# Performance work log

Hardware: AMD Instinct MI355X
Metric: run time of the kernel (lower is better)

The kernel has to match this reference:

```python
import jax, jax.numpy as jnp
import numpy as np

B, N, H, E = 8, 256, 128, 32

def setup_inputs() -> dict:
    key = jax.random.key(0)
    ks = jax.random.split(key, 9)
    x = jax.random.normal(ks[0], (B, N, H), dtype=jnp.float32)
    adj = jax.random.randint(ks[1], (B, N, N), 0, 2, dtype=jnp.int32)
    e = jax.random.normal(ks[2], (B, N, N, E), dtype=jnp.float32)
    s = 0.02
    We = jax.random.normal(ks[3], (E, H), dtype=jnp.float32) * s
    be = jax.random.normal(ks[4], (H,), dtype=jnp.float32) * s
    W1 = jax.random.normal(ks[5], (H, 2 * H), dtype=jnp.float32) * s
    b1 = jax.random.normal(ks[6], (2 * H,), dtype=jnp.float32) * s
    W2 = jax.random.normal(ks[7], (2 * H, H), dtype=jnp.float32) * s
    b2 = jax.random.normal(ks[8], (H,), dtype=jnp.float32) * s
    return {"x": x, "adj": adj, "e": e, "We": We, "be": be,
            "W1": W1, "b1": b1, "W2": W2, "b2": b2}

def reference(x, adj, e, We, be, W1, b1, W2, b2):
    # edge projection: [B,N,N,E] -> [B,N,N,H]
    e_h = jnp.einsum('bije,eh->bijh', e, We) + be
    # message m[b,i,j] = relu(x[b,j] + e_h[b,i,j]); mask by adj
    m = jax.nn.relu(x[:, None, :, :] + e_h)
    m = jnp.where((adj != 0)[..., None], m, jnp.zeros((), m.dtype))
    agg = m.sum(axis=2)  # sum over j -> [B,N,H]
    h = agg + x
    out = jax.nn.relu(h @ W1 + b1) @ W2 + b2
    return out
```

## Files before the change

kernel.cpp:

```cpp
#include <hip/hip_runtime.h>
#include <hip/hip_bf16.h>

#define B_ 8
#define N_ 256
#define H_ 128
#define E_ 32
#define XLS_STRIDE 264

typedef __bf16 bf16x8 __attribute__((ext_vector_type(8)));
typedef __bf16 bf16x4 __attribute__((ext_vector_type(4)));
typedef float f32x4 __attribute__((ext_vector_type(4)));

static __device__ __forceinline__ __bf16 f2bf(float f) {
    union { float f; unsigned int u; } a;
    a.f = f;
    const unsigned int r = a.u + 0x7FFFu + ((a.u >> 16) & 1u);
    union { unsigned short s; __bf16 b; } o;
    o.s = (unsigned short)(r >> 16);
    return o.b;
}

#define W1T_OFF  131072
#define W2T_OFF  163840
#define WEBF_OFF 196608

__global__ __launch_bounds__(256) void prep_kernel(
    const float* __restrict__ x, const float* __restrict__ be,
    const float* __restrict__ W1, const float* __restrict__ W2,
    const float* __restrict__ We, float* __restrict__ ws)
{
    const int blk = blockIdx.x;
    if (blk == 320) {
        __bf16* Webf = (__bf16*)(ws + WEBF_OFF);
        for (int q = threadIdx.x; q < 512; q += 256) {
            const int quad = q >> 7, h = q & 127;
            bf16x8 t;
#pragma unroll
            for (int kk = 0; kk < 8; ++kk)
                t[kk] = f2bf(We[(quad * 8 + kk) * H_ + h]);
            *(bf16x8*)&Webf[q * 8] = t;
        }
        return;
    }
    __shared__ float tile[32][33];
    const int tx = threadIdx.x & 31, ty = threadIdx.x >> 5;
    if (blk < 256) {
        const int b = blk >> 5, t = blk & 31;
        const float* src = x + (size_t)b * N_ * H_;
        __bf16* dst = (__bf16*)ws + (size_t)b * H_ * N_;
        const int r0 = (t >> 2) * 32, c0 = (t & 3) * 32;
#pragma unroll
        for (int p = 0; p < 4; ++p)
            tile[ty + p * 8][tx] =
                src[(size_t)(r0 + ty + p * 8) * H_ + c0 + tx] + be[c0 + tx];
        __syncthreads();
#pragma unroll
        for (int p = 0; p < 4; ++p)
            dst[(size_t)(c0 + ty + p * 8) * N_ + r0 + tx] = f2bf(tile[tx][ty + p * 8]);
        return;
    }
    const float* src; float* dst; int R, C, r0, c0;
    if (blk < 288) {
        const int t = blk - 256;
        src = W1; dst = ws + W1T_OFF;
        R = 128; C = 256; r0 = (t >> 3) * 32; c0 = (t & 7) * 32;
    } else {
        const int t = blk - 288;
        src = W2; dst = ws + W2T_OFF;
        R = 256; C = 128; r0 = (t >> 2) * 32; c0 = (t & 3) * 32;
    }
#pragma unroll
    for (int p = 0; p < 4; ++p)
        tile[ty + p * 8][tx] = src[(size_t)(r0 + ty + p * 8) * C + c0 + tx];
    __syncthreads();
#pragma unroll
    for (int p = 0; p < 4; ++p)
        dst[(size_t)(c0 + ty + p * 8) * R + r0 + tx] = tile[tx][ty + p * 8];
}

__global__ __launch_bounds__(256, 2) void agg_kernel(
    const int* __restrict__ adj, const float* __restrict__ e,
    const float* __restrict__ ws, const float* __restrict__ x,
    float* __restrict__ hout)
{
    __shared__ __bf16 xls[H_ * XLS_STRIDE];
    __shared__ float red[4][128];
    const int bi   = blockIdx.x;
    const int b    = bi >> 8;
    const int tid  = threadIdx.x;
    const int w    = tid >> 6;
    const int lane = tid & 63;
    const int quad = lane >> 4;
    const int col  = lane & 15;

    const size_t ebase   = (size_t)bi * (N_ * E_);
    const size_t adjbase = (size_t)bi * N_;

    float4 a0v[2], a1v[2];
    int4   avv[2];
#pragma unroll
    for (int p = 0; p < 2; ++p) {
        const int j0 = (p * 4 + w) * 16;
        const float* ap = e + ebase + (size_t)(j0 + col) * E_ + quad * 8;
        a0v[p] = *(const float4*)ap;
        a1v[p] = *(const float4*)(ap + 4);
        avv[p] = *(const int4*)(adj + adjbase + j0 + quad * 4);
    }

    {
        const __bf16* gx = (const __bf16*)ws + (size_t)b * (H_ * N_);
#pragma unroll 4
        for (int it = 0; it < 16; ++it) {
            const int k   = it * 256 + tid;
            const int row = k >> 5, cc = k & 31;
            const f32x4 v = *(const f32x4*)(gx + (size_t)row * 256 + cc * 8);
            *(f32x4*)&xls[row * XLS_STRIDE + cc * 8] = v;
        }
    }

    const __bf16* Webf = (const __bf16*)(ws + WEBF_OFF);
    bf16x8 bw[8];
#pragma unroll
    for (int ht = 0; ht < 8; ++ht)
        bw[ht] = *(const bf16x8*)&Webf[(quad * 128 + ht * 16 + col) * 8];

    float psum[8];
#pragma unroll
    for (int ht = 0; ht < 8; ++ht) psum[ht] = 0.0f;

    const f32x4 zero4 = {0.0f, 0.0f, 0.0f, 0.0f};

    __syncthreads();

#pragma unroll
    for (int c = 0; c < 4; ++c) {
        const int s  = c & 1;
        const int jr = (c * 4 + w) * 16 + quad * 4;

        bf16x8 af;
        af[0] = f2bf(a0v[s].x); af[1] = f2bf(a0v[s].y);
        af[2] = f2bf(a0v[s].z); af[3] = f2bf(a0v[s].w);
        af[4] = f2bf(a1v[s].x); af[5] = f2bf(a1v[s].y);
        af[6] = f2bf(a1v[s].z); af[7] = f2bf(a1v[s].w);
        float adjf[4];
        adjf[0] = avv[s].x ? 1.0f : 0.0f;
        adjf[1] = avv[s].y ? 1.0f : 0.0f;
        adjf[2] = avv[s].z ? 1.0f : 0.0f;
        adjf[3] = avv[s].w ? 1.0f : 0.0f;

        if (c < 2) {
            const int j0n = ((c + 2) * 4 + w) * 16;
            const float* apn = e + ebase + (size_t)(j0n + col) * E_ + quad * 8;
            a0v[s] = *(const float4*)apn;
            a1v[s] = *(const float4*)(apn + 4);
            avv[s] = *(const int4*)(adj + adjbase + j0n + quad * 4);
        }

#pragma unroll
        for (int g = 0; g < 2; ++g) {
            f32x4 acc[4];
#pragma unroll
            for (int t = 0; t < 4; ++t)
                acc[t] = __builtin_amdgcn_mfma_f32_16x16x32_bf16(af, bw[g * 4 + t], zero4, 0, 0, 0);
#pragma unroll
            for (int t = 0; t < 4; ++t) {
                const int ht = g * 4 + t;
                const bf16x4 xv = *(const bf16x4*)&xls[(ht * 16 + col) * XLS_STRIDE + jr];
#pragma unroll
                for (int r = 0; r < 4; ++r)
                    psum[ht] += adjf[r] * fmaxf(acc[t][r] + (float)xv[r], 0.0f);
            }
        }
    }

#pragma unroll
    for (int ht = 0; ht < 8; ++ht) {
        float v = psum[ht];
        v += __shfl_xor(v, 16);
        v += __shfl_xor(v, 32);
        if (lane < 16) red[w][ht * 16 + lane] = v;
    }
    __syncthreads();
    if (tid < 128) {
        const float aggv = red[0][tid] + red[1][tid] + red[2][tid] + red[3][tid];
        hout[(size_t)bi * H_ + tid] = aggv + x[(size_t)bi * H_ + tid];
    }
}

__global__ __launch_bounds__(256) void mlp_kernel(
    const float* __restrict__ ws, const float* __restrict__ b1,
    const float* __restrict__ b2, float* __restrict__ hio)
{
    __shared__ float hs[8][128];
    __shared__ float ts[8][256];
    __shared__ float part[8][2][128];
    const int tid = threadIdx.x;
    const int r0  = blockIdx.x * 8;

    ((f32x4*)hs)[tid] = ((const f32x4*)(hio + (size_t)r0 * H_))[tid];
    __syncthreads();

    {
        const float* wrow = ws + W1T_OFF + (size_t)tid * 128;
        float acc[8] = {0.f, 0.f, 0.f, 0.f, 0.f, 0.f, 0.f, 0.f};
        for (int k = 0; k < 128; k += 4) {
            const f32x4 wv = *(const f32x4*)&wrow[k];
#pragma unroll
            for (int r = 0; r < 8; ++r) {
                const f32x4 hv = *(const f32x4*)&hs[r][k];
                acc[r] += hv[0] * wv[0] + hv[1] * wv[1] + hv[2] * wv[2] + hv[3] * wv[3];
            }
        }
        const float bb = b1[tid];
#pragma unroll
        for (int r = 0; r < 8; ++r) ts[r][tid] = fmaxf(acc[r] + bb, 0.0f);
    }
    __syncthreads();

    {
        const int c  = tid & 127;
        const int kb = (tid >> 7) * 128;
        const float* wrow = ws + W2T_OFF + (size_t)c * 256 + kb;
        float acc[8] = {0.f, 0.f, 0.f, 0.f, 0.f, 0.f, 0.f, 0.f};
        for (int k = 0; k < 128; k += 4) {
            const f32x4 wv = *(const f32x4*)&wrow[k];
#pragma unroll
            for (int r = 0; r < 8; ++r) {
                const f32x4 tv = *(const f32x4*)&ts[r][kb + k];
                acc[r] += tv[0] * wv[0] + tv[1] * wv[1] + tv[2] * wv[2] + tv[3] * wv[3];
            }
        }
#pragma unroll
        for (int r = 0; r < 8; ++r) part[r][tid >> 7][c] = acc[r];
    }
    __syncthreads();
#pragma unroll
    for (int idx = tid; idx < 1024; idx += 256) {
        const int r = idx >> 7, c = idx & 127;
        hio[(size_t)(r0 + r) * H_ + c] = part[r][0][c] + part[r][1][c] + b2[c];
    }
}

extern "C" void kernel_launch(void* const* d_in, const int* in_sizes, int n_in,
                              void* d_out, int out_size, void* d_ws, size_t ws_size,
                              hipStream_t stream) {
    const float* x   = (const float*)d_in[0];
    const int*   adj = (const int*)  d_in[1];
    const float* e   = (const float*)d_in[2];
    const float* We  = (const float*)d_in[3];
    const float* be  = (const float*)d_in[4];
    const float* W1  = (const float*)d_in[5];
    const float* b1  = (const float*)d_in[6];
    const float* W2  = (const float*)d_in[7];
    const float* b2  = (const float*)d_in[8];
    float* out = (float*)d_out;
    float* ws  = (float*)d_ws;

    prep_kernel<<<dim3(321), dim3(256), 0, stream>>>(x, be, W1, W2, We, ws);
    agg_kernel<<<dim3(B_ * N_), dim3(256), 0, stream>>>(adj, e, ws, x, out);
    mlp_kernel<<<dim3(B_ * N_ / 8), dim3(256), 0, stream>>>(ws, b1, b2, out);
}
```

Baseline: 143.0 us.

## Drop weight transposes in prep and read W1/W2 directly with split-K MLP

The prep kernel no longer transposes W1 and W2 into the workspace. The MLP kernel now reads the original row-major weights with coalesced per-column loads and runs with 512 threads, splitting K across thread groups and reducing partial sums through shared memory. The f2bf helper is replaced by the compiler's native bf16 conversion. This removes 64 prep blocks and the workspace round trip for the weights, at the cost of an extra reduction pass and sync inside the MLP.

```diff
diff --git a/kernel.cpp b/kernel.cpp
--- a/kernel.cpp
+++ b/kernel.cpp
@@ -12,25 +12,17 @@
 typedef float f32x4 __attribute__((ext_vector_type(4)));
 
 static __device__ __forceinline__ __bf16 f2bf(float f) {
-    union { float f; unsigned int u; } a;
-    a.f = f;
-    const unsigned int r = a.u + 0x7FFFu + ((a.u >> 16) & 1u);
-    union { unsigned short s; __bf16 b; } o;
-    o.s = (unsigned short)(r >> 16);
-    return o.b;
-}
-
-#define W1T_OFF  131072
-#define W2T_OFF  163840
+    return (__bf16)f;
+}
+
 #define WEBF_OFF 196608
 
 __global__ __launch_bounds__(256) void prep_kernel(
     const float* __restrict__ x, const float* __restrict__ be,
-    const float* __restrict__ W1, const float* __restrict__ W2,
     const float* __restrict__ We, float* __restrict__ ws)
 {
     const int blk = blockIdx.x;
-    if (blk == 320) {
+    if (blk == 256) {
         __bf16* Webf = (__bf16*)(ws + WEBF_OFF);
         for (int q = threadIdx.x; q < 512; q += 256) {
             const int quad = q >> 7, h = q & 127;
@@ -44,38 +36,18 @@
     }
     __shared__ float tile[32][33];
     const int tx = threadIdx.x & 31, ty = threadIdx.x >> 5;
-    if (blk < 256) {
-        const int b = blk >> 5, t = blk & 31;
-        const float* src = x + (size_t)b * N_ * H_;
-        __bf16* dst = (__bf16*)ws + (size_t)b * H_ * N_;
-        const int r0 = (t >> 2) * 32, c0 = (t & 3) * 32;
-#pragma unroll
-        for (int p = 0; p < 4; ++p)
-            tile[ty + p * 8][tx] =
-                src[(size_t)(r0 + ty + p * 8) * H_ + c0 + tx] + be[c0 + tx];
-        __syncthreads();
-#pragma unroll
-        for (int p = 0; p < 4; ++p)
-            dst[(size_t)(c0 + ty + p * 8) * N_ + r0 + tx] = f2bf(tile[tx][ty + p * 8]);
-        return;
-    }
-    const float* src; float* dst; int R, C, r0, c0;
-    if (blk < 288) {
-        const int t = blk - 256;
-        src = W1; dst = ws + W1T_OFF;
-        R = 128; C = 256; r0 = (t >> 3) * 32; c0 = (t & 7) * 32;
-    } else {
-        const int t = blk - 288;
-        src = W2; dst = ws + W2T_OFF;
-        R = 256; C = 128; r0 = (t >> 2) * 32; c0 = (t & 3) * 32;
-    }
+    const int b = blk >> 5, t = blk & 31;
+    const float* src = x + (size_t)b * N_ * H_;
+    __bf16* dst = (__bf16*)ws + (size_t)b * H_ * N_;
+    const int r0 = (t >> 2) * 32, c0 = (t & 3) * 32;
 #pragma unroll
     for (int p = 0; p < 4; ++p)
-        tile[ty + p * 8][tx] = src[(size_t)(r0 + ty + p * 8) * C + c0 + tx];
+        tile[ty + p * 8][tx] =
+            src[(size_t)(r0 + ty + p * 8) * H_ + c0 + tx] + be[c0 + tx];
     __syncthreads();
 #pragma unroll
     for (int p = 0; p < 4; ++p)
-        dst[(size_t)(c0 + ty + p * 8) * R + r0 + tx] = tile[tx][ty + p * 8];
+        dst[(size_t)(c0 + ty + p * 8) * N_ + r0 + tx] = f2bf(tile[tx][ty + p * 8]);
 }
 
 __global__ __launch_bounds__(256, 2) void agg_kernel(
@@ -187,57 +159,75 @@
     }
 }
 
-__global__ __launch_bounds__(256) void mlp_kernel(
-    const float* __restrict__ ws, const float* __restrict__ b1,
-    const float* __restrict__ b2, float* __restrict__ hio)
+__global__ __launch_bounds__(512) void mlp_kernel(
+    const float* __restrict__ W1, const float* __restrict__ b1,
+    const float* __restrict__ W2, const float* __restrict__ b2,
+    float* __restrict__ hio)
 {
     __shared__ float hs[8][128];
     __shared__ float ts[8][256];
-    __shared__ float part[8][2][128];
+    __shared__ float part[4096];
     const int tid = threadIdx.x;
     const int r0  = blockIdx.x * 8;
 
-    ((f32x4*)hs)[tid] = ((const f32x4*)(hio + (size_t)r0 * H_))[tid];
+    if (tid < 256)
+        ((f32x4*)hs)[tid] = ((const f32x4*)(hio + (size_t)r0 * H_))[tid];
     __syncthreads();
 
     {
-        const float* wrow = ws + W1T_OFF + (size_t)tid * 128;
+        const int c1 = tid & 255, kh = tid >> 8;
+        const float* wp = W1 + (size_t)(kh * 64) * 256 + c1;
         float acc[8] = {0.f, 0.f, 0.f, 0.f, 0.f, 0.f, 0.f, 0.f};
-        for (int k = 0; k < 128; k += 4) {
-            const f32x4 wv = *(const f32x4*)&wrow[k];
+#pragma unroll 4
+        for (int k = 0; k < 64; k += 4) {
+            const float w0 = wp[(k + 0) * 256];
+            const float w1 = wp[(k + 1) * 256];
+            const float w2 = wp[(k + 2) * 256];
+            const float w3 = wp[(k + 3) * 256];
 #pragma unroll
             for (int r = 0; r < 8; ++r) {
-                const f32x4 hv = *(const f32x4*)&hs[r][k];
-                acc[r] += hv[0] * wv[0] + hv[1] * wv[1] + hv[2] * wv[2] + hv[3] * wv[3];
+                const f32x4 hv = *(const f32x4*)&hs[r][kh * 64 + k];
+                acc[r] += hv[0] * w0 + hv[1] * w1 + hv[2] * w2 + hv[3] * w3;
             }
         }
-        const float bb = b1[tid];
-#pragma unroll
-        for (int r = 0; r < 8; ++r) ts[r][tid] = fmaxf(acc[r] + bb, 0.0f);
+#pragma unroll
+        for (int r = 0; r < 8; ++r) part[(r * 2 + kh) * 256 + c1] = acc[r];
+    }
+    __syncthreads();
+#pragma unroll
+    for (int idx = tid; idx < 2048; idx += 512) {
+        const int r = idx >> 8, c = idx & 255;
+        ts[r][c] = fmaxf(part[(r * 2 + 0) * 256 + c] + part[(r * 2 + 1) * 256 + c]
+                         + b1[c], 0.0f);
     }
     __syncthreads();
 
     {
-        const int c  = tid & 127;
-        const int kb = (tid >> 7) * 128;
-        const float* wrow = ws + W2T_OFF + (size_t)c * 256 + kb;
+        const int c2 = tid & 127, kq = tid >> 7;
+        const float* wp = W2 + (size_t)(kq * 64) * 128 + c2;
         float acc[8] = {0.f, 0.f, 0.f, 0.f, 0.f, 0.f, 0.f, 0.f};
-        for (int k = 0; k < 128; k += 4) {
-            const f32x4 wv = *(const f32x4*)&wrow[k];
+#pragma unroll 4
+        for (int k = 0; k < 64; k += 4) {
+            const float w0 = wp[(k + 0) * 128];
+            const float w1 = wp[(k + 1) * 128];
+            const float w2 = wp[(k + 2) * 128];
+            const float w3 = wp[(k + 3) * 128];
 #pragma unroll
             for (int r = 0; r < 8; ++r) {
-                const f32x4 tv = *(const f32x4*)&ts[r][kb + k];
-                acc[r] += tv[0] * wv[0] + tv[1] * wv[1] + tv[2] * wv[2] + tv[3] * wv[3];
+                const f32x4 tv = *(const f32x4*)&ts[r][kq * 64 + k];
+                acc[r] += tv[0] * w0 + tv[1] * w1 + tv[2] * w2 + tv[3] * w3;
             }
         }
 #pragma unroll
-        for (int r = 0; r < 8; ++r) part[r][tid >> 7][c] = acc[r];
-    }
-    __syncthreads();
-#pragma unroll
-    for (int idx = tid; idx < 1024; idx += 256) {
+        for (int r = 0; r < 8; ++r) part[(r * 4 + kq) * 128 + c2] = acc[r];
+    }
+    __syncthreads();
+#pragma unroll
+    for (int idx = tid; idx < 1024; idx += 512) {
         const int r = idx >> 7, c = idx & 127;
-        hio[(size_t)(r0 + r) * H_ + c] = part[r][0][c] + part[r][1][c] + b2[c];
+        hio[(size_t)(r0 + r) * H_ + c] =
+            part[(r * 4 + 0) * 128 + c] + part[(r * 4 + 1) * 128 + c] +
+            part[(r * 4 + 2) * 128 + c] + part[(r * 4 + 3) * 128 + c] + b2[c];
     }
 }
 
@@ -256,7 +246,7 @@
     float* out = (float*)d_out;
     float* ws  = (float*)d_ws;
 
-    prep_kernel<<<dim3(321), dim3(256), 0, stream>>>(x, be, W1, W2, We, ws);
+    prep_kernel<<<dim3(257), dim3(256), 0, stream>>>(x, be, We, ws);
     agg_kernel<<<dim3(B_ * N_), dim3(256), 0, stream>>>(adj, e, ws, x, out);
-    mlp_kernel<<<dim3(B_ * N_ / 8), dim3(256), 0, stream>>>(ws, b1, b2, out);
-}
+    mlp_kernel<<<dim3(B_ * N_ / 8), dim3(512), 0, stream>>>(W1, b1, W2, b2, out);
+}
```

After: 137.7 us. 3.7% less time.
